# Kernel optimization log

Measured on AMD Instinct MI355X. Metric: run time of the kernel, lower is better.

The kernel has to match this reference:

```python
import jax, jax.numpy as jnp
import numpy as np

NUM_USERS = 60000
NUM_ITEMS = 40000
N_NODES = NUM_USERS + NUM_ITEMS
EMBED_K = 128
E_HALF = 1_000_000  # bipartite interactions; symmetrized -> 2M directed edges


def setup_inputs() -> dict:
    key = jax.random.key(0)
    k1, k2, k3, k4, k5, k6, k7 = jax.random.split(key, 7)
    scale = 1.0 / np.sqrt(EMBED_K)  # ~ xavier_normal
    Gu = jax.random.normal(k1, (NUM_USERS, EMBED_K), jnp.float32) * scale
    Gi = jax.random.normal(k2, (NUM_ITEMS, EMBED_K), jnp.float32) * scale
    W0 = jax.random.normal(k3, (EMBED_K, EMBED_K), jnp.float32) * scale
    W1 = jax.random.normal(k4, (EMBED_K, EMBED_K), jnp.float32) * scale
    W2 = jax.random.normal(k5, (EMBED_K, EMBED_K), jnp.float32) * scale
    # bipartite user-item graph, symmetrized (items offset by NUM_USERS)
    u = jax.random.randint(k6, (E_HALF,), 0, NUM_USERS)
    it = jax.random.randint(k7, (E_HALF,), 0, NUM_ITEMS) + NUM_USERS
    src = jnp.concatenate([u, it])
    dst = jnp.concatenate([it, u])
    edge_index = jnp.stack([src, dst]).astype(jnp.int32)  # [2, 2M]
    return {"Gu": Gu, "Gi": Gi, "W0": W0, "W1": W1, "W2": W2,
            "edge_index": edge_index}


def reference(Gu, Gi, W0, W1, W2, edge_index):
    # add_self_loops=False, bias=False) -> ReLU), then split into (gu, gi).
    src, dst = edge_index[0], edge_index[1]
    n_users = Gu.shape[0]
    n_nodes = Gu.shape[0] + Gi.shape[0]
    # PyG gcn_norm (no self loops): deg = scatter(1, col); norm = d^-1/2[row]*d^-1/2[col]
    ones = jnp.ones(src.shape, Gu.dtype)
    deg = jax.ops.segment_sum(ones, dst, num_segments=n_nodes)
    dinv = jnp.where(deg > 0, jax.lax.rsqrt(jnp.maximum(deg, 1.0)), 0.0)
    norm = dinv[src] * dinv[dst]  # [E]
    x = jnp.concatenate([Gu, Gi], axis=0)  # [N, d]
    for W in (W0, W1, W2):
        h = x @ W                                   # [N, d] dense GEMM
        msg = h[src] * norm[:, None]                # [E, d] gather + scale
        x = jax.nn.relu(jax.ops.segment_sum(msg, dst, num_segments=n_nodes))
    return x[:n_users], x[n_users:]
```

## Files before the change

### kernel.cpp

```cpp
#include <hip/hip_runtime.h>
#include <hip/hip_bf16.h>

#define EMB 128
#define NPB 256
#define NB_PAD 512
#define CHUNK 4096
#define FILL_CAP 7168

typedef unsigned int uint32;
typedef unsigned long long uint64;
typedef __attribute__((ext_vector_type(8))) short bf16x8;
typedef __attribute__((ext_vector_type(4))) float f32x4;
typedef __attribute__((ext_vector_type(2))) float f32x2;
typedef __attribute__((ext_vector_type(2))) unsigned int uint32x2;

__device__ __forceinline__ ushort f2bf(float f) {
    uint32 u = __float_as_uint(f);
    return (ushort)((u + 0x7fff + ((u >> 16) & 1)) >> 16);
}
__device__ __forceinline__ uint32 pack_hi2(uint32 u0, uint32 u1) {
    return (u1 & 0xffff0000u) | (u0 >> 16);
}
__device__ __forceinline__ float blo(uint32 u) { return __uint_as_float(u << 16); }
__device__ __forceinline__ float bhi(uint32 u) { return __uint_as_float(u & 0xffff0000u); }


__global__ __launch_bounds__(256) void bucket_count_kernel(
    const int* __restrict__ dst, int* __restrict__ bucket_cnt, int E, int NB) {
    __shared__ int cnt[NB_PAD];
    int t = threadIdx.x;
    long e0 = (long)blockIdx.x * CHUNK;
    int n = E - (int)e0; if (n > CHUNK) n = CHUNK;
    for (int b = t; b < NB_PAD; b += 256) cnt[b] = 0;
    __syncthreads();
    #pragma unroll
    for (int i = 0; i < CHUNK / 256; i++) {
        int idx = t + i * 256;
        if (idx < n) atomicAdd(&cnt[dst[e0 + idx] >> 8], 1);
    }
    __syncthreads();
    for (int b = t; b < NB; b += 256)
        if (cnt[b] > 0) atomicAdd(&bucket_cnt[b], cnt[b]);
}

__global__ void bucket_scan_kernel(const int* __restrict__ bucket_cnt,
                                   int* __restrict__ ebase, int* __restrict__ gcursor,
                                   int NB, int E) {
    __shared__ int sc[512];
    int t = threadIdx.x;
    int v = (t < NB) ? bucket_cnt[t] : 0;
    sc[t] = v;
    __syncthreads();
    for (int off = 1; off < 512; off <<= 1) {
        int u = (t >= off) ? sc[t - off] : 0;
        __syncthreads();
        sc[t] += u;
        __syncthreads();
    }
    if (t < NB) {
        int excl = sc[t] - v;
        ebase[t] = excl;
        gcursor[t] = excl;
    }
    if (t == 0) ebase[NB] = E;
}


__global__ __launch_bounds__(256) void bucket_scatter_kernel(
    const int* __restrict__ src, const int* __restrict__ dst,
    int* __restrict__ gcursor, uint2* __restrict__ ebuf, int E, int NB) {
    __shared__ int cnt[NB_PAD];
    __shared__ int loff[NB_PAD];
    __shared__ int gbase[NB_PAD];
    __shared__ int pos[NB_PAD];
    __shared__ int sc[256];
    __shared__ uint2 stage[CHUNK];
    int t = threadIdx.x;
    long e0 = (long)blockIdx.x * CHUNK;
    int n = E - (int)e0; if (n > CHUNK) n = CHUNK;
    for (int b = t; b < NB_PAD; b += 256) { cnt[b] = 0; pos[b] = 0; }
    __syncthreads();
    int es[CHUNK / 256], ed[CHUNK / 256];
    #pragma unroll
    for (int i = 0; i < CHUNK / 256; i++) {
        int idx = t + i * 256;
        if (idx < n) {
            es[i] = src[e0 + idx];
            ed[i] = dst[e0 + idx];
            atomicAdd(&cnt[ed[i] >> 8], 1);
        }
    }
    __syncthreads();
    int a = cnt[2 * t], b2 = cnt[2 * t + 1];
    sc[t] = a + b2;
    __syncthreads();
    for (int off = 1; off < 256; off <<= 1) {
        int v = (t >= off) ? sc[t - off] : 0;
        __syncthreads();
        sc[t] += v;
        __syncthreads();
    }
    int excl = sc[t] - (a + b2);
    loff[2 * t] = excl;
    loff[2 * t + 1] = excl + a;
    __syncthreads();
    for (int b = t; b < NB; b += 256)
        if (cnt[b] > 0) gbase[b] = atomicAdd(&gcursor[b], cnt[b]);
    __syncthreads();
    #pragma unroll
    for (int i = 0; i < CHUNK / 256; i++) {
        int idx = t + i * 256;
        if (idx < n) {
            int b = ed[i] >> 8;
            int p = atomicAdd(&pos[b], 1);
            stage[loff[b] + p] = make_uint2((uint32)es[i], (uint32)ed[i]);
        }
    }
    __syncthreads();
    for (int b = t; b < NB; b += 256) {
        int c = cnt[b], lo = loff[b], go = gbase[b];
        for (int k = 0; k < c; k++) ebuf[go + k] = stage[lo + k];
    }
}


__global__ __launch_bounds__(256) void bucket_deg_kernel(
    const uint2* __restrict__ ebuf, const int* __restrict__ ebase,
    int* __restrict__ deg, float* __restrict__ dinv, int N) {
    __shared__ int cnt[NPB];
    int t = threadIdx.x;
    int n0 = blockIdx.x * NPB;
    int nn = N - n0; if (nn > NPB) nn = NPB;
    cnt[t] = 0;
    __syncthreads();
    int e0 = ebase[blockIdx.x];
    int e1 = ebase[blockIdx.x + 1];
    for (int e = e0 + t; e < e1; e += 256) {
        uint2 sd = ebuf[e];
        atomicAdd(&cnt[(int)sd.y - n0], 1);
    }
    __syncthreads();
    if (t < nn) {
        int c = cnt[t];
        deg[n0 + t] = c;
        dinv[n0 + t] = c > 0 ? rsqrtf((float)c) : 0.0f;
    }
}


__global__ void scan1_kernel(const int* __restrict__ deg, int* __restrict__ rowptr,
                             int* __restrict__ bsum, int N) {
    __shared__ int sc[256];
    int t = threadIdx.x;
    int base = blockIdx.x * 1024 + t * 4;
    int d0 = 0, d1 = 0, d2 = 0, d3 = 0;
    if (base + 3 < N) {
        int4 v = *(const int4*)(deg + base);
        d0 = v.x; d1 = v.y; d2 = v.z; d3 = v.w;
    } else {
        if (base     < N) d0 = deg[base];
        if (base + 1 < N) d1 = deg[base + 1];
        if (base + 2 < N) d2 = deg[base + 2];
        if (base + 3 < N) d3 = deg[base + 3];
    }
    int s = d0 + d1 + d2 + d3;
    sc[t] = s;
    __syncthreads();
    for (int off = 1; off < 256; off <<= 1) {
        int v = (t >= off) ? sc[t - off] : 0;
        __syncthreads();
        sc[t] += v;
        __syncthreads();
    }
    int excl = sc[t] - s;
    if (t == 255) bsum[blockIdx.x] = sc[255];
    int dd[4] = {d0, d1, d2, d3};
    int p = excl;
    #pragma unroll
    for (int j = 0; j < 4; j++) {
        int i = base + j;
        if (i < N) rowptr[i] = p;
        p += dd[j];
    }
}

__global__ void scan2_kernel(int* bsum, int nb) {
    __shared__ int sc[128];
    int t = threadIdx.x;
    int v = (t < nb) ? bsum[t] : 0;
    sc[t] = v;
    __syncthreads();
    for (int off = 1; off < 128; off <<= 1) {
        int u = (t >= off) ? sc[t - off] : 0;
        __syncthreads();
        sc[t] += u;
        __syncthreads();
    }
    if (t < nb) bsum[t] = sc[t] - v;
}

__global__ void scan3_kernel(int* __restrict__ rowptr, const int* __restrict__ bsum,
                             int N, int E) {
    int t = threadIdx.x, b = blockIdx.x;
    int add = bsum[b];
    int base = b * 1024 + t * 4;
    #pragma unroll
    for (int j = 0; j < 4; j++) {
        int i = base + j;
        if (i < N) rowptr[i] += add;
    }
    if (b == 0 && t == 0) rowptr[N] = E;
}


__global__ __launch_bounds__(256) void fill_ew_kernel(
    uint2* __restrict__ ebuf, const int* __restrict__ rowptr,
    const float* __restrict__ dinv, int N) {
    __shared__ uint2 stage[FILL_CAP];
    __shared__ int cnt[NPB];
    __shared__ int rp[NPB];
    int t = threadIdx.x;
    int n0 = blockIdx.x * NPB;
    int nn = N - n0; if (nn > NPB) nn = NPB;
    if (t < nn) { cnt[t] = 0; rp[t] = rowptr[n0 + t]; }
    __syncthreads();
    int e0 = rowptr[n0];
    int e1 = rowptr[n0 + nn];
    int ecount = e1 - e0; if (ecount > FILL_CAP) ecount = FILL_CAP;
    for (int o = t; o < ecount; o += 256) stage[o] = ebuf[e0 + o];
    __syncthreads();
    for (int o = t; o < ecount; o += 256) {
        uint2 sd = stage[o];
        int local = (int)sd.y - n0;
        int p = atomicAdd(&cnt[local], 1);
        int s = (int)sd.x;
        ebuf[rp[local] + p] = make_uint2((uint32)s, __float_as_uint(dinv[s]));
    }
}


template<int DI>
__device__ __forceinline__ void agg_tail2(
    const uint32x2* __restrict__ Yh2, const uint2* __restrict__ ew,
    int base, int e0, int e1, int half, int l32,
    float& a0, float& a1, float& a2, float& a3) {
    uint32 rows[DI]; float w[DI]; uint32x2 p[DI];
    #pragma unroll
    for (int k = 0; k < DI; k++) {
        int i0 = base + 2 * k, i1 = i0 + 1;
        uint2 s0 = ew[i0 < e1 ? i0 : e0];
        uint2 s1 = ew[i1 < e1 ? i1 : e0];
        rows[k] = half ? s1.x : s0.x;
        uint32 wu = half ? s1.y : s0.y;
        w[k] = (i0 + half < e1) ? __uint_as_float(wu) : 0.0f;
    }
    #pragma unroll
    for (int k = 0; k < DI; k++) p[k] = Yh2[(size_t)rows[k] * 32 + l32];
    #pragma unroll
    for (int k = 0; k < DI; k++) {
        a0 += w[k] * blo(p[k].x); a1 += w[k] * bhi(p[k].x);
        a2 += w[k] * blo(p[k].y); a3 += w[k] * bhi(p[k].y);
    }
}

__device__ __forceinline__ void agg_node2(
    const uint32x2* __restrict__ Yh2, const uint2* __restrict__ ew,
    int e0, int e1, int half, int l32,
    float& a0, float& a1, float& a2, float& a3) {
    int base = e0;
    for (; base + 16 <= e1; base += 16) {
        uint32 rows[8]; float w[8]; uint32x2 p[8];
        #pragma unroll
        for (int k = 0; k < 8; k++) {
            uint2 s0 = ew[base + 2 * k];
            uint2 s1 = ew[base + 2 * k + 1];
            rows[k] = half ? s1.x : s0.x;
            w[k] = __uint_as_float(half ? s1.y : s0.y);
        }
        #pragma unroll
        for (int k = 0; k < 8; k++) p[k] = Yh2[(size_t)rows[k] * 32 + l32];
        #pragma unroll
        for (int k = 0; k < 8; k++) {
            a0 += w[k] * blo(p[k].x); a1 += w[k] * bhi(p[k].x);
            a2 += w[k] * blo(p[k].y); a3 += w[k] * bhi(p[k].y);
        }
    }
    int rem = e1 - base;
    if (rem > 8)      agg_tail2<8>(Yh2, ew, base, e0, e1, half, l32, a0, a1, a2, a3);
    else if (rem > 4) agg_tail2<4>(Yh2, ew, base, e0, e1, half, l32, a0, a1, a2, a3);
    else if (rem > 2) agg_tail2<2>(Yh2, ew, base, e0, e1, half, l32, a0, a1, a2, a3);
    else if (rem > 0) agg_tail2<1>(Yh2, ew, base, e0, e1, half, l32, a0, a1, a2, a3);
}

__global__ __launch_bounds__(256) void agg_relu_kernel(
    const uint32x2* __restrict__ Yh2,
    const int* __restrict__ rowptr, const uint2* __restrict__ ew,
    const float* __restrict__ dinv, float* __restrict__ out, int N) {
    int node = blockIdx.x * 4 + (threadIdx.x >> 6);
    if (node >= N) return;
    int lane = threadIdx.x & 63;
    int half = lane >> 5, l32 = lane & 31;
    int e0 = __builtin_amdgcn_readfirstlane(rowptr[node]);
    int e1 = __builtin_amdgcn_readfirstlane(rowptr[node + 1]);
    float a0 = 0.f, a1 = 0.f, a2 = 0.f, a3 = 0.f;
    agg_node2(Yh2, ew, e0, e1, half, l32, a0, a1, a2, a3);
    a0 += __shfl_xor(a0, 32);
    a1 += __shfl_xor(a1, 32);
    a2 += __shfl_xor(a2, 32);
    a3 += __shfl_xor(a3, 32);
    if (half == 0) {
        float wd = dinv[node];
        f32x4 r = { fmaxf(a0 * wd, 0.f), fmaxf(a1 * wd, 0.f),
                    fmaxf(a2 * wd, 0.f), fmaxf(a3 * wd, 0.f) };
        __builtin_nontemporal_store(r, (f32x4*)(out + (size_t)node * EMB + l32 * 4));
    }
}


__global__ void wsplit_kernel(const float* __restrict__ W0, const float* __restrict__ W1,
                              const float* __restrict__ W2,
                              ushort* __restrict__ Whi, ushort* __restrict__ Wlo) {
    const float* W = (blockIdx.x == 0) ? W0 : (blockIdx.x == 1) ? W1 : W2;
    ushort* hiT = Whi + blockIdx.x * EMB * EMB;
    ushort* loT = Wlo + blockIdx.x * EMB * EMB;
    for (int i = threadIdx.x; i < EMB * EMB; i += blockDim.x) {
        int k = i >> 7, n = i & 127;
        float w = W[i];
        uint32 u = __float_as_uint(w);
        ushort hi = (ushort)(u >> 16);
        float hif = __uint_as_float(u & 0xffff0000u);
        ushort lo = f2bf(w - hif);
        hiT[n * EMB + k] = hi;
        loT[n * EMB + k] = lo;
    }
}


union FragU { uint32 u[4]; bf16x8 v; };

__global__ __launch_bounds__(256, 2) void gemm_mfma_kernel(
    const float* __restrict__ A, const float* __restrict__ A2, int Msplit,
    const ushort* __restrict__ WhiT, const ushort* __restrict__ WloT,
    ushort* __restrict__ Yh, int M) {
    __shared__ float As[16][132];
    int t = threadIdx.x;
    int wv = t >> 6, lane = t & 63, quad = lane >> 4, l16 = lane & 15;

    FragU bfr[8][2];
    #pragma unroll
    for (int kc = 0; kc < 8; kc++) {
        const ushort* srcW = (kc < 4) ? WhiT : WloT;
        int kb = (kc & 3) * 32 + quad * 8;
        #pragma unroll
        for (int c = 0; c < 2; c++) {
            int n = wv * 32 + c * 16 + l16;
            const uint32* p = (const uint32*)(srcW + n * EMB + kb);
            bfr[kc][c].u[0] = p[0];
            bfr[kc][c].u[1] = p[1];
            bfr[kc][c].u[2] = p[2];
            bfr[kc][c].u[3] = p[3];
        }
    }

    int srow = t >> 4, skq = t & 15;
    int ntile = (M + 15) >> 4;
    for (int tile = blockIdx.x; tile < ntile; tile += (int)gridDim.x) {
        int r0 = tile << 4;
        __syncthreads();
        {
            float4 v0 = {0.f, 0.f, 0.f, 0.f}, v1 = v0;
            int row = r0 + srow;
            if (row < M) {
                const float* ga = (row < Msplit)
                    ? A  + (size_t)row * EMB + skq * 8
                    : A2 + (size_t)(row - Msplit) * EMB + skq * 8;
                v0 = *(const float4*)ga;
                v1 = *(const float4*)(ga + 4);
            }
            *(float4*)&As[srow][skq * 8] = v0;
            *(float4*)&As[srow][skq * 8 + 4] = v1;
        }
        __syncthreads();

        FragU ah[4], al[4];
        #pragma unroll
        for (int kc = 0; kc < 4; kc++) {
            const float* p = &As[l16][kc * 32 + quad * 8];
            float4 xa = *(const float4*)p;
            float4 xb = *(const float4*)(p + 4);
            uint32 u0 = __float_as_uint(xa.x), u1 = __float_as_uint(xa.y);
            uint32 u2 = __float_as_uint(xa.z), u3 = __float_as_uint(xa.w);
            uint32 u4 = __float_as_uint(xb.x), u5 = __float_as_uint(xb.y);
            uint32 u6 = __float_as_uint(xb.z), u7 = __float_as_uint(xb.w);
            ah[kc].u[0] = pack_hi2(u0, u1);
            ah[kc].u[1] = pack_hi2(u2, u3);
            ah[kc].u[2] = pack_hi2(u4, u5);
            ah[kc].u[3] = pack_hi2(u6, u7);
            float l0 = xa.x - __uint_as_float(u0 & 0xffff0000u);
            float l1 = xa.y - __uint_as_float(u1 & 0xffff0000u);
            float l2 = xa.z - __uint_as_float(u2 & 0xffff0000u);
            float l3 = xa.w - __uint_as_float(u3 & 0xffff0000u);
            float l4 = xb.x - __uint_as_float(u4 & 0xffff0000u);
            float l5 = xb.y - __uint_as_float(u5 & 0xffff0000u);
            float l6 = xb.z - __uint_as_float(u6 & 0xffff0000u);
            float l7 = xb.w - __uint_as_float(u7 & 0xffff0000u);
            al[kc].u[0] = pack_hi2(__float_as_uint(l0), __float_as_uint(l1));
            al[kc].u[1] = pack_hi2(__float_as_uint(l2), __float_as_uint(l3));
            al[kc].u[2] = pack_hi2(__float_as_uint(l4), __float_as_uint(l5));
            al[kc].u[3] = pack_hi2(__float_as_uint(l6), __float_as_uint(l7));
        }

        f32x4 acc0 = {0.f, 0.f, 0.f, 0.f};
        f32x4 acc1 = {0.f, 0.f, 0.f, 0.f};
        #pragma unroll
        for (int kc = 0; kc < 4; kc++) {
            acc0 = __builtin_amdgcn_mfma_f32_16x16x32_bf16(ah[kc].v, bfr[kc][0].v, acc0, 0, 0, 0);
            acc1 = __builtin_amdgcn_mfma_f32_16x16x32_bf16(ah[kc].v, bfr[kc][1].v, acc1, 0, 0, 0);
        }
        #pragma unroll
        for (int kc = 0; kc < 4; kc++) {
            acc0 = __builtin_amdgcn_mfma_f32_16x16x32_bf16(ah[kc].v, bfr[kc + 4][0].v, acc0, 0, 0, 0);
            acc1 = __builtin_amdgcn_mfma_f32_16x16x32_bf16(ah[kc].v, bfr[kc + 4][1].v, acc1, 0, 0, 0);
        }
        #pragma unroll
        for (int kc = 0; kc < 4; kc++) {
            acc0 = __builtin_amdgcn_mfma_f32_16x16x32_bf16(al[kc].v, bfr[kc][0].v, acc0, 0, 0, 0);
            acc1 = __builtin_amdgcn_mfma_f32_16x16x32_bf16(al[kc].v, bfr[kc][1].v, acc1, 0, 0, 0);
        }

        int colb = wv * 32 + l16;
        #pragma unroll
        for (int r = 0; r < 4; r++) {
            int row = r0 + quad * 4 + r;
            if (row < M) {
                Yh[(size_t)row * EMB + colb]      = f2bf(acc0[r]);
                Yh[(size_t)row * EMB + colb + 16] = f2bf(acc1[r]);
            }
        }
    }
}


extern "C" void kernel_launch(void* const* d_in, const int* in_sizes, int n_in,
                              void* d_out, int out_size, void* d_ws, size_t ws_size,
                              hipStream_t stream) {
    (void)n_in; (void)out_size; (void)ws_size;
    const float* Gu = (const float*)d_in[0];
    const float* Gi = (const float*)d_in[1];
    const float* W0 = (const float*)d_in[2];
    const float* W1 = (const float*)d_in[3];
    const float* W2 = (const float*)d_in[4];
    const int* ei = (const int*)d_in[5];

    int nu = in_sizes[0] / EMB;
    int ni = in_sizes[1] / EMB;
    int N = nu + ni;
    int E = in_sizes[5] / 2;
    const int* src = ei;
    const int* dst = ei + E;
    int NB = (N + NPB - 1) / NPB;

    ushort* Yh      = (ushort*)d_ws;
    uint2* ebuf     = (uint2*)(Yh + (size_t)N * EMB);
    int* deg        = (int*)(ebuf + (size_t)E);
    int* rowptr     = deg + N;
    float* dinv     = (float*)(rowptr + N + 1);
    int* bucket_cnt = (int*)(dinv + N);
    int* ebase      = bucket_cnt + NB;
    int* gcursor    = ebase + NB + 1;
    int* bsum       = gcursor + NB;
    ushort* WhiT    = (ushort*)(bsum + 128);
    ushort* WloT    = WhiT + 3 * EMB * EMB;
    float* X        = (float*)d_out;

    (void)hipMemsetAsync(bucket_cnt, 0, sizeof(int) * (size_t)NB, stream);

    wsplit_kernel<<<3, 256, 0, stream>>>(W0, W1, W2, WhiT, WloT);

    int ecb = (E + CHUNK - 1) / CHUNK;
    bucket_count_kernel<<<ecb, 256, 0, stream>>>(dst, bucket_cnt, E, NB);
    bucket_scan_kernel<<<1, 512, 0, stream>>>(bucket_cnt, ebase, gcursor, NB, E);
    bucket_scatter_kernel<<<ecb, 256, 0, stream>>>(src, dst, gcursor, ebuf, E, NB);
    bucket_deg_kernel<<<NB, 256, 0, stream>>>(ebuf, ebase, deg, dinv, N);
    int nb = (N + 1023) / 1024;
    scan1_kernel<<<nb, 256, 0, stream>>>(deg, rowptr, bsum, N);
    scan2_kernel<<<1, 128, 0, stream>>>(bsum, nb);
    scan3_kernel<<<nb, 256, 0, stream>>>(rowptr, bsum, N, E);
    fill_ew_kernel<<<NB, 256, 0, stream>>>(ebuf, rowptr, dinv, N);

    const uint2* ew = (const uint2*)ebuf;
    int aggBlocks = (N + 3) / 4;
    const int GB = 512;

    gemm_mfma_kernel<<<GB, 256, 0, stream>>>(Gu, Gi, nu, WhiT, WloT, Yh, N);
    agg_relu_kernel<<<aggBlocks, 256, 0, stream>>>((const uint32x2*)Yh, rowptr, ew, dinv, X, N);
    gemm_mfma_kernel<<<GB, 256, 0, stream>>>(X, X, N, WhiT + EMB * EMB, WloT + EMB * EMB, Yh, N);
    agg_relu_kernel<<<aggBlocks, 256, 0, stream>>>((const uint32x2*)Yh, rowptr, ew, dinv, X, N);
    gemm_mfma_kernel<<<GB, 256, 0, stream>>>(X, X, N, WhiT + 2 * EMB * EMB, WloT + 2 * EMB * EMB, Yh, N);
    agg_relu_kernel<<<aggBlocks, 256, 0, stream>>>((const uint32x2*)Yh, rowptr, ew, dinv, X, N);
}
```

Before: 470.2 us.

## Fuse degree counting into bucket count, drop bucket_deg kernel, improve scatter copy

Degree counting moves into bucket_count_kernel as global atomics on deg, so the separate bucket_deg pass over the edge buffer goes away. dinv is now computed inside scan1. The scatter's final copy from shared staging to global memory changes from a serial per-bucket loop to a flat thread-strided loop. fill_ew batches four edges per thread so more loads are in flight. The cost is 2M global atomics on deg, with contention that depends on node degree.

```diff
diff --git a/kernel.cpp b/kernel.cpp
--- a/kernel.cpp
+++ b/kernel.cpp
@@ -26,7 +26,8 @@
 
 
 __global__ __launch_bounds__(256) void bucket_count_kernel(
-    const int* __restrict__ dst, int* __restrict__ bucket_cnt, int E, int NB) {
+    const int* __restrict__ dst, int* __restrict__ bucket_cnt,
+    int* __restrict__ deg, int E, int NB) {
     __shared__ int cnt[NB_PAD];
     int t = threadIdx.x;
     long e0 = (long)blockIdx.x * CHUNK;
@@ -36,7 +37,11 @@
     #pragma unroll
     for (int i = 0; i < CHUNK / 256; i++) {
         int idx = t + i * 256;
-        if (idx < n) atomicAdd(&cnt[dst[e0 + idx] >> 8], 1);
+        if (idx < n) {
+            int d = dst[e0 + idx];
+            atomicAdd(&cnt[d >> 8], 1);
+            atomicAdd(&deg[d], 1);
+        }
     }
     __syncthreads();
     for (int b = t; b < NB; b += 256)
@@ -117,39 +122,16 @@
         }
     }
     __syncthreads();
-    for (int b = t; b < NB; b += 256) {
-        int c = cnt[b], lo = loff[b], go = gbase[b];
-        for (int k = 0; k < c; k++) ebuf[go + k] = stage[lo + k];
-    }
-}
-
-
-__global__ __launch_bounds__(256) void bucket_deg_kernel(
-    const uint2* __restrict__ ebuf, const int* __restrict__ ebase,
-    int* __restrict__ deg, float* __restrict__ dinv, int N) {
-    __shared__ int cnt[NPB];
-    int t = threadIdx.x;
-    int n0 = blockIdx.x * NPB;
-    int nn = N - n0; if (nn > NPB) nn = NPB;
-    cnt[t] = 0;
-    __syncthreads();
-    int e0 = ebase[blockIdx.x];
-    int e1 = ebase[blockIdx.x + 1];
-    for (int e = e0 + t; e < e1; e += 256) {
-        uint2 sd = ebuf[e];
-        atomicAdd(&cnt[(int)sd.y - n0], 1);
-    }
-    __syncthreads();
-    if (t < nn) {
-        int c = cnt[t];
-        deg[n0 + t] = c;
-        dinv[n0 + t] = c > 0 ? rsqrtf((float)c) : 0.0f;
+    for (int i = t; i < n; i += 256) {
+        uint2 e = stage[i];
+        int b = (int)e.y >> 8;
+        ebuf[gbase[b] + (i - loff[b])] = e;
     }
 }
 
 
 __global__ void scan1_kernel(const int* __restrict__ deg, int* __restrict__ rowptr,
-                             int* __restrict__ bsum, int N) {
+                             int* __restrict__ bsum, float* __restrict__ dinv, int N) {
     __shared__ int sc[256];
     int t = threadIdx.x;
     int base = blockIdx.x * 1024 + t * 4;
@@ -179,7 +161,10 @@
     #pragma unroll
     for (int j = 0; j < 4; j++) {
         int i = base + j;
-        if (i < N) rowptr[i] = p;
+        if (i < N) {
+            rowptr[i] = p;
+            dinv[i] = dd[j] > 0 ? rsqrtf((float)dd[j]) : 0.0f;
+        }
         p += dd[j];
     }
 }
@@ -229,12 +214,26 @@
     int ecount = e1 - e0; if (ecount > FILL_CAP) ecount = FILL_CAP;
     for (int o = t; o < ecount; o += 256) stage[o] = ebuf[e0 + o];
     __syncthreads();
-    for (int o = t; o < ecount; o += 256) {
-        uint2 sd = stage[o];
-        int local = (int)sd.y - n0;
-        int p = atomicAdd(&cnt[local], 1);
-        int s = (int)sd.x;
-        ebuf[rp[local] + p] = make_uint2((uint32)s, __float_as_uint(dinv[s]));
+    for (int o = t; o < ecount; o += 1024) {
+        uint2 sd[4]; int pos[4]; float wv[4];
+        int valid = 0;
+        #pragma unroll
+        for (int k = 0; k < 4; k++) {
+            int oo = o + k * 256;
+            if (oo < ecount) { sd[k] = stage[oo]; valid = k + 1; }
+        }
+        #pragma unroll
+        for (int k = 0; k < 4; k++)
+            if (k < valid) {
+                int local = (int)sd[k].y - n0;
+                pos[k] = rp[local] + atomicAdd(&cnt[local], 1);
+            }
+        #pragma unroll
+        for (int k = 0; k < 4; k++)
+            if (k < valid) wv[k] = dinv[(int)sd[k].x];
+        #pragma unroll
+        for (int k = 0; k < 4; k++)
+            if (k < valid) ebuf[pos[k]] = make_uint2(sd[k].x, __float_as_uint(wv[k]));
     }
 }
 
@@ -463,27 +462,26 @@
     ushort* Yh      = (ushort*)d_ws;
     uint2* ebuf     = (uint2*)(Yh + (size_t)N * EMB);
     int* deg        = (int*)(ebuf + (size_t)E);
-    int* rowptr     = deg + N;
+    int* bucket_cnt = deg + N;
+    int* rowptr     = bucket_cnt + NB;
     float* dinv     = (float*)(rowptr + N + 1);
-    int* bucket_cnt = (int*)(dinv + N);
-    int* ebase      = bucket_cnt + NB;
+    int* ebase      = (int*)(dinv + N);
     int* gcursor    = ebase + NB + 1;
     int* bsum       = gcursor + NB;
     ushort* WhiT    = (ushort*)(bsum + 128);
     ushort* WloT    = WhiT + 3 * EMB * EMB;
     float* X        = (float*)d_out;
 
-    (void)hipMemsetAsync(bucket_cnt, 0, sizeof(int) * (size_t)NB, stream);
+    (void)hipMemsetAsync(deg, 0, sizeof(int) * (size_t)(N + NB), stream);
 
     wsplit_kernel<<<3, 256, 0, stream>>>(W0, W1, W2, WhiT, WloT);
 
     int ecb = (E + CHUNK - 1) / CHUNK;
-    bucket_count_kernel<<<ecb, 256, 0, stream>>>(dst, bucket_cnt, E, NB);
+    bucket_count_kernel<<<ecb, 256, 0, stream>>>(dst, bucket_cnt, deg, E, NB);
     bucket_scan_kernel<<<1, 512, 0, stream>>>(bucket_cnt, ebase, gcursor, NB, E);
     bucket_scatter_kernel<<<ecb, 256, 0, stream>>>(src, dst, gcursor, ebuf, E, NB);
-    bucket_deg_kernel<<<NB, 256, 0, stream>>>(ebuf, ebase, deg, dinv, N);
     int nb = (N + 1023) / 1024;
-    scan1_kernel<<<nb, 256, 0, stream>>>(deg, rowptr, bsum, N);
+    scan1_kernel<<<nb, 256, 0, stream>>>(deg, rowptr, bsum, dinv, N);
     scan2_kernel<<<1, 128, 0, stream>>>(bsum, nb);
     scan3_kernel<<<nb, 256, 0, stream>>>(rowptr, bsum, N, E);
     fill_ew_kernel<<<NB, 256, 0, stream>>>(ebuf, rowptr, dinv, N);
```

Result: slower. 535.1 us (+13.8%).
